# Kernel tuning notes

Hardware: AMD Instinct MI355X
Metric: run time of the kernel (lower is better)

The kernel has to match this reference:

```python
import jax, jax.numpy as jnp
import numpy as np

N_NODES = 100000
LAYER_NUM = 3


def gcn_conv(x, src, dst, W, b, n):
    # PyG GCNConv: add self-loops, symmetric normalization D^-1/2 (A+I) D^-1/2, x@W, +b
    h = x @ W                                   # [N, out]
    ones = jnp.ones(src.shape[0], dtype=h.dtype)
    deg = jax.ops.segment_sum(ones, dst, num_segments=n) + 1.0  # +1 for self-loop
    dinv = jax.lax.rsqrt(deg)                   # deg >= 1 always (self-loop)
    norm = dinv[src] * dinv[dst]                # [E]
    msgs = h[src] * norm[:, None]               # gather + scale, [E, out]
    agg = jax.ops.segment_sum(msgs, dst, num_segments=n)
    agg = agg + h * (dinv * dinv)[:, None]      # self-loop contribution
    return agg + b


def setup_inputs() -> dict:
    key = jax.random.key(0)
    ks = jax.random.split(key, 8)
    in_d, mid_d, out_d = 512, 256, 40
    n, e = N_NODES, 1600000
    x = jax.random.normal(ks[0], (n, in_d), dtype=jnp.float32)
    edge_index = jax.random.randint(ks[1], (2, e), 0, n, dtype=jnp.int64)
    def glorot(k, fan_in, fan_out):
        s = jnp.sqrt(6.0 / (fan_in + fan_out))
        return jax.random.uniform(k, (fan_in, fan_out), jnp.float32, -s, s)
    W1 = glorot(ks[2], in_d, mid_d)
    b1 = jnp.zeros((mid_d,), jnp.float32)
    Wi = glorot(ks[3], mid_d, mid_d)
    bi = jnp.zeros((mid_d,), jnp.float32)
    W2 = glorot(ks[4], mid_d, out_d)
    b2 = jnp.zeros((out_d,), jnp.float32)
    return {"x": x, "edge_index": edge_index, "W1": W1, "b1": b1,
            "Wi": Wi, "bi": bi, "W2": W2, "b2": b2}


def reference(x, edge_index, W1, b1, Wi, bi, W2, b2):
    n = x.shape[0]
    src, dst = edge_index[0], edge_index[1]
    h = gcn_conv(x, src, dst, W1, b1, n)
    for _ in range(LAYER_NUM):
        h = gcn_conv(h, src, dst, Wi, bi, n)
        h = jax.nn.relu(h)
    emb = h  # detached embedding in original
    h = jax.nn.relu(h)
    h = gcn_conv(h, src, dst, W2, b2, n)
    return (jax.nn.log_softmax(h, axis=1), emb)
```

## Files before the change

### kernel.cpp

```cpp
#include <hip/hip_runtime.h>
#include <cmath>

typedef __attribute__((ext_vector_type(8))) short short8v;
typedef __attribute__((ext_vector_type(4))) short short4v;
typedef __attribute__((ext_vector_type(4))) float f32x4;

__device__ inline short f2bf(float f) {
  union { float f; unsigned u; } a; a.f = f;
  unsigned r = a.u + 0x7FFF + ((a.u >> 16) & 1);
  return (short)(r >> 16);
}
__device__ inline float bf2f(short b) {
  union { unsigned u; float f; } a; a.u = ((unsigned)(unsigned short)b) << 16;
  return a.f;
}

__global__ void count_deg_kernel(const int* __restrict__ dst, int* __restrict__ deg, int e) {
  int i = blockIdx.x * blockDim.x + threadIdx.x;
  int stride = gridDim.x * blockDim.x;
  for (; i < e; i += stride) atomicAdd(&deg[dst[i]], 1);
}

__global__ void dinv_kernel(const int* __restrict__ deg, float* __restrict__ dinv, int n) {
  int i = blockIdx.x * blockDim.x + threadIdx.x;
  if (i < n) dinv[i] = rsqrtf((float)deg[i] + 1.0f);
}

#define SCAN_T 1024
__global__ void scan_blocks_kernel(const int* __restrict__ deg, int* __restrict__ rs,
                                   int* __restrict__ bsum, int n) {
  __shared__ int s[SCAN_T];
  int t = threadIdx.x;
  int i = blockIdx.x * SCAN_T + t;
  int own = (i < n) ? deg[i] : 0;
  s[t] = own;
  for (int off = 1; off < SCAN_T; off <<= 1) {
    __syncthreads();
    int add = (t >= off) ? s[t - off] : 0;
    __syncthreads();
    s[t] += add;
  }
  if (i < n) rs[i] = s[t] - own;
  if (t == SCAN_T - 1) bsum[blockIdx.x] = s[t];
}

__global__ void scan_bsum_kernel(int* __restrict__ bsum, int nb) {
  __shared__ int s[128];
  int t = threadIdx.x;
  int v = (t < nb) ? bsum[t] : 0;
  s[t] = v;
  for (int off = 1; off < 128; off <<= 1) {
    __syncthreads();
    int add = (t >= off) ? s[t - off] : 0;
    __syncthreads();
    s[t] += add;
  }
  if (t < nb) bsum[t] = s[t] - v;
}

__global__ void add_off_kernel(int* __restrict__ rs, const int* __restrict__ bsum, int n) {
  int i = blockIdx.x * blockDim.x + threadIdx.x;
  if (i < n) rs[i] += bsum[i >> 10];
}

__global__ void fill_csr_kernel(const int* __restrict__ src, const int* __restrict__ dst,
                                const int* __restrict__ rs, int* __restrict__ cursor,
                                int* __restrict__ col, int e) {
  int i = blockIdx.x * blockDim.x + threadIdx.x;
  int stride = gridDim.x * blockDim.x;
  for (; i < e; i += stride) {
    int d = dst[i];
    int p = rs[d] + atomicAdd(&cursor[d], 1);
    col[p] = src[i];
  }
}

__global__ void convert_wt_kernel(const float* __restrict__ W, short* __restrict__ Wt,
                                  int K, int N) {
  int i = blockIdx.x * blockDim.x + threadIdx.x;
  if (i < K * N) {
    int k = i / N, nn = i - k * N;
    Wt[nn * K + k] = f2bf(W[i]);
  }
}

__global__ void convert_w2t_kernel(const float* __restrict__ W2, short* __restrict__ W2t) {
  int i = blockIdx.x * blockDim.x + threadIdx.x;
  if (i < 64 * 256) {
    int c = i >> 8, k = i & 255;
    W2t[i] = (c < 40) ? f2bf(W2[k * 40 + c]) : (short)0;
  }
}

template <int K, bool AF32>
__global__ __launch_bounds__(256, 3) void gemm_mfma_kernel(
    const void* __restrict__ Aptr, const short* __restrict__ Wt,
    const float* __restrict__ dinv, char* __restrict__ G8,
    float* __restrict__ gscale, int n) {
  __shared__ short As[64 * 64];
  __shared__ short Bs[256 * 64];
  __shared__ float rmax[4][64];
  int tid = threadIdx.x;
  int lane = tid & 63, wid = tid >> 6;
  int wn = wid;
  int l15 = lane & 15, lh = lane >> 4;
  int rowBase = blockIdx.x * 64;

  f32x4 acc[4][4];
#pragma unroll
  for (int mi = 0; mi < 4; mi++)
#pragma unroll
    for (int ni = 0; ni < 4; ni++) acc[mi][ni] = (f32x4){0.f, 0.f, 0.f, 0.f};

  for (int kt = 0; kt < K; kt += 64) {
#pragma unroll
    for (int i = 0; i < 2; i++) {
      int s = tid + i * 256;
      int r = s >> 3, u = s & 7;
      int gr = rowBase + r; if (gr >= n) gr = n - 1;
      short8v v;
      if constexpr (AF32) {
        const float* ap = (const float*)Aptr + (size_t)gr * K + kt + u * 8;
        float4 f0 = *(const float4*)ap;
        float4 f1 = *(const float4*)(ap + 4);
        v[0] = f2bf(f0.x); v[1] = f2bf(f0.y); v[2] = f2bf(f0.z); v[3] = f2bf(f0.w);
        v[4] = f2bf(f1.x); v[5] = f2bf(f1.y); v[6] = f2bf(f1.z); v[7] = f2bf(f1.w);
      } else {
        v = *(const short8v*)((const short*)Aptr + (size_t)gr * K + kt + u * 8);
      }
      *(short8v*)&As[r * 64 + ((u ^ (r & 7)) << 3)] = v;
    }
#pragma unroll
    for (int i = 0; i < 8; i++) {
      int s = tid + i * 256;
      int r = s >> 3, u = s & 7;
      short8v v = *(const short8v*)(Wt + (size_t)r * K + kt + u * 8);
      *(short8v*)&Bs[r * 64 + ((u ^ (r & 7)) << 3)] = v;
    }
    __syncthreads();
#pragma unroll
    for (int kk = 0; kk < 2; kk++) {
      int u = kk * 4 + lh;
      short8v af[4], bf[4];
#pragma unroll
      for (int mi = 0; mi < 4; mi++) {
        int r = mi * 16 + l15;
        af[mi] = *(const short8v*)&As[r * 64 + ((u ^ (r & 7)) << 3)];
      }
#pragma unroll
      for (int ni = 0; ni < 4; ni++) {
        int r = wn * 64 + ni * 16 + l15;
        bf[ni] = *(const short8v*)&Bs[r * 64 + ((u ^ (r & 7)) << 3)];
      }
#pragma unroll
      for (int mi = 0; mi < 4; mi++)
#pragma unroll
        for (int ni = 0; ni < 4; ni++)
          acc[mi][ni] = __builtin_amdgcn_mfma_f32_16x16x32_bf16(
              af[mi], bf[ni], acc[mi][ni], 0, 0, 0);
    }
    __syncthreads();
  }

#pragma unroll
  for (int mi = 0; mi < 4; mi++) {
#pragma unroll
    for (int j = 0; j < 4; j++) {
      float mx = 0.f;
#pragma unroll
      for (int ni = 0; ni < 4; ni++) mx = fmaxf(mx, fabsf(acc[mi][ni][j]));
      for (int off = 1; off < 16; off <<= 1)
        mx = fmaxf(mx, __shfl_xor(mx, off, 64));
      if (l15 == 0) rmax[wn][mi * 16 + lh * 4 + j] = mx;
    }
  }
  __syncthreads();
#pragma unroll
  for (int mi = 0; mi < 4; mi++) {
#pragma unroll
    for (int j = 0; j < 4; j++) {
      int r = mi * 16 + lh * 4 + j;
      int gr = rowBase + r;
      if (gr < n) {
        float cmax = fmaxf(fmaxf(rmax[0][r], rmax[1][r]),
                           fmaxf(rmax[2][r], rmax[3][r]));
        float inv = (cmax > 0.f) ? 127.f / cmax : 0.f;
        if (wn == 0 && l15 == 0)
          gscale[gr] = dinv[gr] * cmax * (1.f / 127.f);
#pragma unroll
        for (int ni = 0; ni < 4; ni++) {
          int gc = wn * 64 + ni * 16 + l15;
          int q = (int)rintf(acc[mi][ni][j] * inv);
          G8[(size_t)gr * 256 + gc] = (char)q;
        }
      }
    }
  }
}

__global__ __launch_bounds__(256, 3) void gemm_mfma40_kernel(
    const short* __restrict__ Hb, const short* __restrict__ W2t,
    const float* __restrict__ dinv, short* __restrict__ G2b, int n) {
  __shared__ short As[256 * 64];
  __shared__ short Bs[64 * 64];
  int tid = threadIdx.x;
  int lane = tid & 63, wid = tid >> 6;
  int l15 = lane & 15, lh = lane >> 4;
  int rowBase = blockIdx.x * 256;

  f32x4 acc[4][4];
#pragma unroll
  for (int mi = 0; mi < 4; mi++)
#pragma unroll
    for (int ni = 0; ni < 4; ni++) acc[mi][ni] = (f32x4){0.f, 0.f, 0.f, 0.f};

  for (int kt = 0; kt < 256; kt += 64) {
#pragma unroll
    for (int i = 0; i < 8; i++) {
      int s = tid + i * 256;
      int r = s >> 3, u = s & 7;
      int gr = rowBase + r; if (gr >= n) gr = n - 1;
      short8v v = *(const short8v*)(Hb + (size_t)gr * 256 + kt + u * 8);
      *(short8v*)&As[r * 64 + ((u ^ (r & 7)) << 3)] = v;
    }
#pragma unroll
    for (int i = 0; i < 2; i++) {
      int s = tid + i * 256;
      int r = s >> 3, u = s & 7;
      short8v v = *(const short8v*)(W2t + (size_t)r * 256 + kt + u * 8);
      *(short8v*)&Bs[r * 64 + ((u ^ (r & 7)) << 3)] = v;
    }
    __syncthreads();
#pragma unroll
    for (int kk = 0; kk < 2; kk++) {
      int u = kk * 4 + lh;
      short8v af[4], bf[4];
#pragma unroll
      for (int mi = 0; mi < 4; mi++) {
        int r = wid * 64 + mi * 16 + l15;
        af[mi] = *(const short8v*)&As[r * 64 + ((u ^ (r & 7)) << 3)];
      }
#pragma unroll
      for (int ni = 0; ni < 4; ni++) {
        int r = ni * 16 + l15;
        bf[ni] = *(const short8v*)&Bs[r * 64 + ((u ^ (r & 7)) << 3)];
      }
#pragma unroll
      for (int mi = 0; mi < 4; mi++)
#pragma unroll
        for (int ni = 0; ni < 4; ni++)
          acc[mi][ni] = __builtin_amdgcn_mfma_f32_16x16x32_bf16(
              af[mi], bf[ni], acc[mi][ni], 0, 0, 0);
    }
    __syncthreads();
  }

#pragma unroll
  for (int mi = 0; mi < 4; mi++) {
#pragma unroll
    for (int j = 0; j < 4; j++) {
      int gr = rowBase + wid * 64 + mi * 16 + lh * 4 + j;
      if (gr < n) {
        float sc = dinv[gr];
#pragma unroll
        for (int ni = 0; ni < 4; ni++) {
          int gc = ni * 16 + l15;
          if (gc < 40) G2b[(size_t)gr * 40 + gc] = f2bf(acc[mi][ni][j] * sc);
        }
      }
    }
  }
}

__device__ inline void dq_acc(int w, float s, float& a0, float& a1,
                              float& a2, float& a3) {
  a0 += (float)(signed char)(w & 0xff) * s;
  a1 += (float)(signed char)((w >> 8) & 0xff) * s;
  a2 += (float)(signed char)((w >> 16) & 0xff) * s;
  a3 += (float)(signed char)(w >> 24) * s;
}

template <int RELU, int WF32>
__global__ __launch_bounds__(256) void aggregate_i8_kernel(
    const char* __restrict__ G8, const float* __restrict__ gsc,
    const int* __restrict__ col, const int* __restrict__ rs,
    const int* __restrict__ deg, const float* __restrict__ dinv,
    const float* __restrict__ bias, short* __restrict__ Hb,
    float* __restrict__ Hf, int n) {
  int wid = threadIdx.x >> 6;
  int lane = threadIdx.x & 63;
  int v = blockIdx.x * 4 + wid;
  if (v >= n) return;
  float a0 = 0.f, a1 = 0.f, a2 = 0.f, a3 = 0.f;
  {
    int w = *(const int*)(G8 + (size_t)v * 256 + lane * 4);
    dq_acc(w, gsc[v], a0, a1, a2, a3);
  }
  int base = rs[v], cnt = deg[v];
  for (int i0 = 0; i0 < cnt; i0 += 64) {
    int rem = cnt - i0; if (rem > 64) rem = 64;
    int ci = col[base + i0 + (lane < rem ? lane : 0)];
    int i = 0;
    for (; i + 8 <= rem; i += 8) {
      int u0 = __shfl(ci, i + 0), u1 = __shfl(ci, i + 1);
      int u2 = __shfl(ci, i + 2), u3 = __shfl(ci, i + 3);
      int u4 = __shfl(ci, i + 4), u5 = __shfl(ci, i + 5);
      int u6 = __shfl(ci, i + 6), u7 = __shfl(ci, i + 7);
      int w0 = *(const int*)(G8 + (size_t)u0 * 256 + lane * 4);
      int w1 = *(const int*)(G8 + (size_t)u1 * 256 + lane * 4);
      int w2 = *(const int*)(G8 + (size_t)u2 * 256 + lane * 4);
      int w3 = *(const int*)(G8 + (size_t)u3 * 256 + lane * 4);
      int w4 = *(const int*)(G8 + (size_t)u4 * 256 + lane * 4);
      int w5 = *(const int*)(G8 + (size_t)u5 * 256 + lane * 4);
      int w6 = *(const int*)(G8 + (size_t)u6 * 256 + lane * 4);
      int w7 = *(const int*)(G8 + (size_t)u7 * 256 + lane * 4);
      float s0 = gsc[u0], s1 = gsc[u1], s2 = gsc[u2], s3 = gsc[u3];
      float s4 = gsc[u4], s5 = gsc[u5], s6 = gsc[u6], s7 = gsc[u7];
      dq_acc(w0, s0, a0, a1, a2, a3);
      dq_acc(w1, s1, a0, a1, a2, a3);
      dq_acc(w2, s2, a0, a1, a2, a3);
      dq_acc(w3, s3, a0, a1, a2, a3);
      dq_acc(w4, s4, a0, a1, a2, a3);
      dq_acc(w5, s5, a0, a1, a2, a3);
      dq_acc(w6, s6, a0, a1, a2, a3);
      dq_acc(w7, s7, a0, a1, a2, a3);
    }
    for (; i < rem; i++) {
      int u = __shfl(ci, i);
      int w = *(const int*)(G8 + (size_t)u * 256 + lane * 4);
      dq_acc(w, gsc[u], a0, a1, a2, a3);
    }
  }
  float s = dinv[v];
  float4 b4 = ((const float4*)bias)[lane];
  float o0 = a0 * s + b4.x, o1 = a1 * s + b4.y, o2 = a2 * s + b4.z, o3 = a3 * s + b4.w;
  if (RELU) {
    o0 = fmaxf(o0, 0.f); o1 = fmaxf(o1, 0.f);
    o2 = fmaxf(o2, 0.f); o3 = fmaxf(o3, 0.f);
  }
  short4v ob; ob[0] = f2bf(o0); ob[1] = f2bf(o1); ob[2] = f2bf(o2); ob[3] = f2bf(o3);
  *(short4v*)(Hb + (size_t)v * 256 + lane * 4) = ob;
  if (WF32) {
    float4 of; of.x = o0; of.y = o1; of.z = o2; of.w = o3;
    *(float4*)(Hf + (size_t)v * 256 + lane * 4) = of;
  }
}

__global__ __launch_bounds__(256) void agg40_lsm_kernel(
    const short* __restrict__ G2b, const int* __restrict__ col,
    const int* __restrict__ rs, const int* __restrict__ deg,
    const float* __restrict__ dinv, const float* __restrict__ b2,
    float* __restrict__ out, int n) {
  int wid = threadIdx.x >> 6;
  int lane = threadIdx.x & 63;
  int v = blockIdx.x * 4 + wid;
  if (v >= n) return;
  bool act = lane < 40;
  int ln = act ? lane : 0;
  float acc = act ? bf2f(G2b[(size_t)v * 40 + lane]) : 0.f;
  int base = rs[v], cnt = deg[v];
  for (int i0 = 0; i0 < cnt; i0 += 64) {
    int rem = cnt - i0; if (rem > 64) rem = 64;
    int ci = col[base + i0 + (lane < rem ? lane : 0)];
    int i = 0;
    for (; i + 4 <= rem; i += 4) {
      int u0 = __shfl(ci, i + 0), u1 = __shfl(ci, i + 1);
      int u2 = __shfl(ci, i + 2), u3 = __shfl(ci, i + 3);
      float x0 = bf2f(G2b[(size_t)u0 * 40 + ln]);
      float x1 = bf2f(G2b[(size_t)u1 * 40 + ln]);
      float x2 = bf2f(G2b[(size_t)u2 * 40 + ln]);
      float x3 = bf2f(G2b[(size_t)u3 * 40 + ln]);
      acc += x0 + x1 + x2 + x3;
    }
    for (; i < rem; i++) {
      int u = __shfl(ci, i);
      acc += bf2f(G2b[(size_t)u * 40 + ln]);
    }
  }
  float val;
  if (act) val = acc * dinv[v] + b2[lane];
  else val = -INFINITY;
  float m = val;
  for (int off = 32; off; off >>= 1) m = fmaxf(m, __shfl_xor(m, off, 64));
  float e = act ? expf(val - m) : 0.f;
  float ssum = e;
  for (int off = 32; off; off >>= 1) ssum += __shfl_xor(ssum, off, 64);
  if (act) out[(size_t)v * 40 + lane] = val - m - logf(ssum);
}


static inline size_t alignup(size_t x) { return (x + 255) & ~(size_t)255; }

extern "C" void kernel_launch(void* const* d_in, const int* in_sizes, int n_in,
                              void* d_out, int out_size, void* d_ws, size_t ws_size,
                              hipStream_t stream) {
  const float* x  = (const float*)d_in[0];
  const int*   ei = (const int*)d_in[1];
  const float* W1 = (const float*)d_in[2];
  const float* b1 = (const float*)d_in[3];
  const float* Wi = (const float*)d_in[4];
  const float* bi = (const float*)d_in[5];
  const float* W2 = (const float*)d_in[6];
  const float* b2 = (const float*)d_in[7];

  const int in_d = 512, mid_d = 256, out_d = 40;
  int n = in_sizes[0] / in_d;
  int E = in_sizes[1] / 2;
  const int* src = ei;
  const int* dst = ei + E;

  float* out_lsm = (float*)d_out;
  float* emb     = (float*)d_out + (size_t)n * out_d;

  char* w = (char*)d_ws;
  float* dinv  = (float*)w;  w += alignup((size_t)n * 4);
  int* deg     = (int*)w;    w += alignup((size_t)n * 4);
  int* rs      = (int*)w;    w += alignup((size_t)n * 4);
  int* cursor  = (int*)w;    w += alignup((size_t)n * 4);
  int* colidx  = (int*)w;    w += alignup((size_t)E * 4);
  int* bsum    = (int*)w;    w += alignup(128 * 4);
  short* W1t   = (short*)w;  w += alignup((size_t)mid_d * in_d * 2);
  short* Wit   = (short*)w;  w += alignup((size_t)mid_d * mid_d * 2);
  short* W2t   = (short*)w;  w += alignup((size_t)64 * mid_d * 2);
  char* G8     = (char*)w;   w += alignup((size_t)n * mid_d);
  float* gsc   = (float*)w;  w += alignup((size_t)n * 4);
  short* Hb    = (short*)w;  w += alignup((size_t)n * mid_d * 2);
  short* G2b   = (short*)G8;

  int nb = (n + SCAN_T - 1) / SCAN_T;

  hipMemsetAsync(deg, 0, (size_t)n * 4, stream);
  hipMemsetAsync(cursor, 0, (size_t)n * 4, stream);
  count_deg_kernel<<<2048, 256, 0, stream>>>(dst, deg, E);
  dinv_kernel<<<(n + 255) / 256, 256, 0, stream>>>(deg, dinv, n);
  scan_blocks_kernel<<<nb, SCAN_T, 0, stream>>>(deg, rs, bsum, n);
  scan_bsum_kernel<<<1, 128, 0, stream>>>(bsum, nb);
  add_off_kernel<<<(n + 255) / 256, 256, 0, stream>>>(rs, bsum, n);
  fill_csr_kernel<<<2048, 256, 0, stream>>>(src, dst, rs, cursor, colidx, E);

  convert_wt_kernel<<<(in_d * mid_d + 255) / 256, 256, 0, stream>>>(W1, W1t, in_d, mid_d);
  convert_wt_kernel<<<(mid_d * mid_d + 255) / 256, 256, 0, stream>>>(Wi, Wit, mid_d, mid_d);
  convert_w2t_kernel<<<(64 * mid_d + 255) / 256, 256, 0, stream>>>(W2, W2t);

  int ggrid = (n + 63) / 64;
  int agg_grid = (n + 3) / 4;

  gemm_mfma_kernel<512, true><<<ggrid, 256, 0, stream>>>(x, W1t, dinv, G8, gsc, n);
  aggregate_i8_kernel<0, 0><<<agg_grid, 256, 0, stream>>>(
      G8, gsc, colidx, rs, deg, dinv, b1, Hb, nullptr, n);
  for (int l = 0; l < 2; l++) {
    gemm_mfma_kernel<256, false><<<ggrid, 256, 0, stream>>>(Hb, Wit, dinv, G8, gsc, n);
    aggregate_i8_kernel<1, 0><<<agg_grid, 256, 0, stream>>>(
        G8, gsc, colidx, rs, deg, dinv, bi, Hb, nullptr, n);
  }
  gemm_mfma_kernel<256, false><<<ggrid, 256, 0, stream>>>(Hb, Wit, dinv, G8, gsc, n);
  aggregate_i8_kernel<1, 1><<<agg_grid, 256, 0, stream>>>(
      G8, gsc, colidx, rs, deg, dinv, bi, Hb, emb, n);

  gemm_mfma40_kernel<<<(n + 255) / 256, 256, 0, stream>>>(Hb, W2t, dinv, G2b, n);
  agg40_lsm_kernel<<<agg_grid, 256, 0, stream>>>(G2b, colidx, rs, deg, dinv, b2, out_lsm, n);
}
```

Measured before the change: 771.3 us.

## Sort neighbor indices per wave and split int8 gather across half-waves

Each aggregation kernel now sorts the chunk of neighbor indices with an in-wave bitonic network before gathering, aiming for more local memory accesses. The int8 aggregation kernel also has each half-wave load 8 bytes per lane from alternate neighbors and combines the halves with a cross-half shuffle, halving the number of gather instructions per edge. The sort adds many shuffle stages per chunk, which may outweigh any locality gain for low-degree nodes.

```diff
diff --git a/kernel.cpp b/kernel.cpp
--- a/kernel.cpp
+++ b/kernel.cpp
@@ -13,6 +13,22 @@
 __device__ inline float bf2f(short b) {
   union { unsigned u; float f; } a; a.u = ((unsigned)(unsigned short)b) << 16;
   return a.f;
+}
+
+__device__ inline int bitonic64(int key, int lane) {
+#pragma unroll
+  for (int k = 2; k <= 64; k <<= 1) {
+#pragma unroll
+    for (int j = k >> 1; j > 0; j >>= 1) {
+      int y = __shfl_xor(key, j, 64);
+      bool lower = (lane & j) == 0;
+      bool asc = (lane & k) == 0;
+      int mn = key < y ? key : y;
+      int mx = key < y ? y : key;
+      key = (lower == asc) ? mn : mx;
+    }
+  }
+  return key;
 }
 
 __global__ void count_deg_kernel(const int* __restrict__ dst, int* __restrict__ deg, int e) {
@@ -272,12 +288,16 @@
   }
 }
 
-__device__ inline void dq_acc(int w, float s, float& a0, float& a1,
-                              float& a2, float& a3) {
-  a0 += (float)(signed char)(w & 0xff) * s;
-  a1 += (float)(signed char)((w >> 8) & 0xff) * s;
-  a2 += (float)(signed char)((w >> 16) & 0xff) * s;
-  a3 += (float)(signed char)(w >> 24) * s;
+__device__ inline void acc8(uint2 w, float s, float* a) {
+  int x = (int)w.x, y = (int)w.y;
+  a[0] += (float)(signed char)(x & 0xff) * s;
+  a[1] += (float)(signed char)((x >> 8) & 0xff) * s;
+  a[2] += (float)(signed char)((x >> 16) & 0xff) * s;
+  a[3] += (float)(signed char)(x >> 24) * s;
+  a[4] += (float)(signed char)(y & 0xff) * s;
+  a[5] += (float)(signed char)((y >> 8) & 0xff) * s;
+  a[6] += (float)(signed char)((y >> 16) & 0xff) * s;
+  a[7] += (float)(signed char)(y >> 24) * s;
 }
 
 template <int RELU, int WF32>
@@ -289,60 +309,79 @@
     float* __restrict__ Hf, int n) {
   int wid = threadIdx.x >> 6;
   int lane = threadIdx.x & 63;
+  int half = lane >> 5;
+  int hl = lane & 31;
   int v = blockIdx.x * 4 + wid;
   if (v >= n) return;
-  float a0 = 0.f, a1 = 0.f, a2 = 0.f, a3 = 0.f;
+
+  float a[8];
+#pragma unroll
+  for (int j = 0; j < 8; j++) a[j] = 0.f;
+
   {
-    int w = *(const int*)(G8 + (size_t)v * 256 + lane * 4);
-    dq_acc(w, gsc[v], a0, a1, a2, a3);
-  }
+    uint2 w = *(const uint2*)(G8 + (size_t)v * 256 + hl * 8);
+    float s = half ? 0.f : gsc[v];
+    acc8(w, s, a);
+  }
+
   int base = rs[v], cnt = deg[v];
   for (int i0 = 0; i0 < cnt; i0 += 64) {
     int rem = cnt - i0; if (rem > 64) rem = 64;
     int ci = col[base + i0 + (lane < rem ? lane : 0)];
+    int key = (lane < rem) ? ci : 0x7FFFFFFF;
+    key = bitonic64(key, lane);
     int i = 0;
     for (; i + 8 <= rem; i += 8) {
-      int u0 = __shfl(ci, i + 0), u1 = __shfl(ci, i + 1);
-      int u2 = __shfl(ci, i + 2), u3 = __shfl(ci, i + 3);
-      int u4 = __shfl(ci, i + 4), u5 = __shfl(ci, i + 5);
-      int u6 = __shfl(ci, i + 6), u7 = __shfl(ci, i + 7);
-      int w0 = *(const int*)(G8 + (size_t)u0 * 256 + lane * 4);
-      int w1 = *(const int*)(G8 + (size_t)u1 * 256 + lane * 4);
-      int w2 = *(const int*)(G8 + (size_t)u2 * 256 + lane * 4);
-      int w3 = *(const int*)(G8 + (size_t)u3 * 256 + lane * 4);
-      int w4 = *(const int*)(G8 + (size_t)u4 * 256 + lane * 4);
-      int w5 = *(const int*)(G8 + (size_t)u5 * 256 + lane * 4);
-      int w6 = *(const int*)(G8 + (size_t)u6 * 256 + lane * 4);
-      int w7 = *(const int*)(G8 + (size_t)u7 * 256 + lane * 4);
+      int u0 = __shfl(key, i + 0 + half);
+      int u1 = __shfl(key, i + 2 + half);
+      int u2 = __shfl(key, i + 4 + half);
+      int u3 = __shfl(key, i + 6 + half);
       float s0 = gsc[u0], s1 = gsc[u1], s2 = gsc[u2], s3 = gsc[u3];
-      float s4 = gsc[u4], s5 = gsc[u5], s6 = gsc[u6], s7 = gsc[u7];
-      dq_acc(w0, s0, a0, a1, a2, a3);
-      dq_acc(w1, s1, a0, a1, a2, a3);
-      dq_acc(w2, s2, a0, a1, a2, a3);
-      dq_acc(w3, s3, a0, a1, a2, a3);
-      dq_acc(w4, s4, a0, a1, a2, a3);
-      dq_acc(w5, s5, a0, a1, a2, a3);
-      dq_acc(w6, s6, a0, a1, a2, a3);
-      dq_acc(w7, s7, a0, a1, a2, a3);
-    }
-    for (; i < rem; i++) {
-      int u = __shfl(ci, i);
-      int w = *(const int*)(G8 + (size_t)u * 256 + lane * 4);
-      dq_acc(w, gsc[u], a0, a1, a2, a3);
-    }
-  }
-  float s = dinv[v];
-  float4 b4 = ((const float4*)bias)[lane];
-  float o0 = a0 * s + b4.x, o1 = a1 * s + b4.y, o2 = a2 * s + b4.z, o3 = a3 * s + b4.w;
+      uint2 w0 = *(const uint2*)(G8 + (size_t)u0 * 256 + hl * 8);
+      uint2 w1 = *(const uint2*)(G8 + (size_t)u1 * 256 + hl * 8);
+      uint2 w2 = *(const uint2*)(G8 + (size_t)u2 * 256 + hl * 8);
+      uint2 w3 = *(const uint2*)(G8 + (size_t)u3 * 256 + hl * 8);
+      acc8(w0, s0, a);
+      acc8(w1, s1, a);
+      acc8(w2, s2, a);
+      acc8(w3, s3, a);
+    }
+    for (; i < rem; i += 2) {
+      int idx = i + half;
+      bool ok = idx < rem;
+      int u = __shfl(key, ok ? idx : i);
+      float s = ok ? gsc[u] : 0.f;
+      uint2 w = *(const uint2*)(G8 + (size_t)u * 256 + hl * 8);
+      acc8(w, s, a);
+    }
+  }
+
+#pragma unroll
+  for (int j = 0; j < 8; j++) a[j] += __shfl_xor(a[j], 32, 64);
+
+  float sc = dinv[v];
+  const float4* bp = (const float4*)(bias + hl * 8);
+  float4 b0 = bp[0], b1 = bp[1];
+  float o[8];
+  o[0] = a[0] * sc + b0.x; o[1] = a[1] * sc + b0.y;
+  o[2] = a[2] * sc + b0.z; o[3] = a[3] * sc + b0.w;
+  o[4] = a[4] * sc + b1.x; o[5] = a[5] * sc + b1.y;
+  o[6] = a[6] * sc + b1.z; o[7] = a[7] * sc + b1.w;
   if (RELU) {
-    o0 = fmaxf(o0, 0.f); o1 = fmaxf(o1, 0.f);
-    o2 = fmaxf(o2, 0.f); o3 = fmaxf(o3, 0.f);
-  }
-  short4v ob; ob[0] = f2bf(o0); ob[1] = f2bf(o1); ob[2] = f2bf(o2); ob[3] = f2bf(o3);
-  *(short4v*)(Hb + (size_t)v * 256 + lane * 4) = ob;
-  if (WF32) {
-    float4 of; of.x = o0; of.y = o1; of.z = o2; of.w = o3;
-    *(float4*)(Hf + (size_t)v * 256 + lane * 4) = of;
+#pragma unroll
+    for (int j = 0; j < 8; j++) o[j] = fmaxf(o[j], 0.f);
+  }
+  if (half == 0) {
+    short8v ob;
+#pragma unroll
+    for (int j = 0; j < 8; j++) ob[j] = f2bf(o[j]);
+    *(short8v*)(Hb + (size_t)v * 256 + hl * 8) = ob;
+  }
+  if (WF32 && half == 1) {
+    float4 f0; f0.x = o[0]; f0.y = o[1]; f0.z = o[2]; f0.w = o[3];
+    float4 f1; f1.x = o[4]; f1.y = o[5]; f1.z = o[6]; f1.w = o[7];
+    *(float4*)(Hf + (size_t)v * 256 + hl * 8) = f0;
+    *(float4*)(Hf + (size_t)v * 256 + hl * 8 + 4) = f1;
   }
 }
 
@@ -362,10 +401,12 @@
   for (int i0 = 0; i0 < cnt; i0 += 64) {
     int rem = cnt - i0; if (rem > 64) rem = 64;
     int ci = col[base + i0 + (lane < rem ? lane : 0)];
+    int key = (lane < rem) ? ci : 0x7FFFFFFF;
+    key = bitonic64(key, lane);
     int i = 0;
     for (; i + 4 <= rem; i += 4) {
-      int u0 = __shfl(ci, i + 0), u1 = __shfl(ci, i + 1);
-      int u2 = __shfl(ci, i + 2), u3 = __shfl(ci, i + 3);
+      int u0 = __shfl(key, i + 0), u1 = __shfl(key, i + 1);
+      int u2 = __shfl(key, i + 2), u3 = __shfl(key, i + 3);
       float x0 = bf2f(G2b[(size_t)u0 * 40 + ln]);
       float x1 = bf2f(G2b[(size_t)u1 * 40 + ln]);
       float x2 = bf2f(G2b[(size_t)u2 * 40 + ln]);
@@ -373,7 +414,7 @@
       acc += x0 + x1 + x2 + x3;
     }
     for (; i < rem; i++) {
-      int u = __shfl(ci, i);
+      int u = __shfl(key, i);
       acc += bf2f(G2b[(size_t)u * 40 + ln]);
     }
   }
```

Result: slower. 860.2 us (+11.5%).

## Prefetch next GEMM K-tile into registers while computing current tile

Applied to the files above, without the earlier changes.

The GEMM main loop now loads the next K-tile of A and W into registers before running the MFMA compute on the current LDS tile, then stores to LDS after a barrier. This is meant to hide global memory latency behind matrix-core work. The register-staged tiles raise register pressure, so launch bounds drop from 3 to 2 blocks per CU, which may reduce occupancy.

```diff
diff --git a/kernel.cpp b/kernel.cpp
--- a/kernel.cpp
+++ b/kernel.cpp
@@ -93,7 +93,7 @@
 }
 
 template <int K, bool AF32>
-__global__ __launch_bounds__(256, 3) void gemm_mfma_kernel(
+__global__ __launch_bounds__(256, 2) void gemm_mfma_kernel(
     const void* __restrict__ Aptr, const short* __restrict__ Wt,
     const float* __restrict__ dinv, char* __restrict__ G8,
     float* __restrict__ gscale, int n) {
@@ -101,8 +101,7 @@
   __shared__ short Bs[256 * 64];
   __shared__ float rmax[4][64];
   int tid = threadIdx.x;
-  int lane = tid & 63, wid = tid >> 6;
-  int wn = wid;
+  int lane = tid & 63, wn = tid >> 6;
   int l15 = lane & 15, lh = lane >> 4;
   int rowBase = blockIdx.x * 64;
 
@@ -112,32 +111,50 @@
 #pragma unroll
     for (int ni = 0; ni < 4; ni++) acc[mi][ni] = (f32x4){0.f, 0.f, 0.f, 0.f};
 
-  for (int kt = 0; kt < K; kt += 64) {
+  short8v aS[2], bS[8];
+
+  auto LOAD = [&](int kt) {
 #pragma unroll
     for (int i = 0; i < 2; i++) {
       int s = tid + i * 256;
       int r = s >> 3, u = s & 7;
       int gr = rowBase + r; if (gr >= n) gr = n - 1;
-      short8v v;
       if constexpr (AF32) {
         const float* ap = (const float*)Aptr + (size_t)gr * K + kt + u * 8;
         float4 f0 = *(const float4*)ap;
         float4 f1 = *(const float4*)(ap + 4);
+        short8v v;
         v[0] = f2bf(f0.x); v[1] = f2bf(f0.y); v[2] = f2bf(f0.z); v[3] = f2bf(f0.w);
         v[4] = f2bf(f1.x); v[5] = f2bf(f1.y); v[6] = f2bf(f1.z); v[7] = f2bf(f1.w);
+        aS[i] = v;
       } else {
-        v = *(const short8v*)((const short*)Aptr + (size_t)gr * K + kt + u * 8);
-      }
-      *(short8v*)&As[r * 64 + ((u ^ (r & 7)) << 3)] = v;
+        aS[i] = *(const short8v*)((const short*)Aptr + (size_t)gr * K + kt + u * 8);
+      }
     }
 #pragma unroll
     for (int i = 0; i < 8; i++) {
       int s = tid + i * 256;
       int r = s >> 3, u = s & 7;
-      short8v v = *(const short8v*)(Wt + (size_t)r * K + kt + u * 8);
-      *(short8v*)&Bs[r * 64 + ((u ^ (r & 7)) << 3)] = v;
-    }
-    __syncthreads();
+      bS[i] = *(const short8v*)(Wt + (size_t)r * K + kt + u * 8);
+    }
+  };
+
+  auto STORE = [&]() {
+#pragma unroll
+    for (int i = 0; i < 2; i++) {
+      int s = tid + i * 256;
+      int r = s >> 3, u = s & 7;
+      *(short8v*)&As[r * 64 + ((u ^ (r & 7)) << 3)] = aS[i];
+    }
+#pragma unroll
+    for (int i = 0; i < 8; i++) {
+      int s = tid + i * 256;
+      int r = s >> 3, u = s & 7;
+      *(short8v*)&Bs[r * 64 + ((u ^ (r & 7)) << 3)] = bS[i];
+    }
+  };
+
+  auto COMPUTE = [&]() {
 #pragma unroll
     for (int kk = 0; kk < 2; kk++) {
       int u = kk * 4 + lh;
@@ -159,8 +176,19 @@
           acc[mi][ni] = __builtin_amdgcn_mfma_f32_16x16x32_bf16(
               af[mi], bf[ni], acc[mi][ni], 0, 0, 0);
     }
-    __syncthreads();
-  }
+  };
+
+  LOAD(0);
+  STORE();
+  __syncthreads();
+  for (int kt = 64; kt < K; kt += 64) {
+    LOAD(kt);
+    COMPUTE();
+    __syncthreads();
+    STORE();
+    __syncthreads();
+  }
+  COMPUTE();
 
 #pragma unroll
   for (int mi = 0; mi < 4; mi++) {
```

New measurement: 775.6 us. No clear change (+0.6%).
